# Optimization experiments

Measured on AMD Instinct MI355X. Metric: run time of the kernel, lower is better.

Reference implementation:

```python
import jax, jax.numpy as jnp
import numpy as np

NUM_EXPERTS = 64
TOP_K = 8
N_TOKENS = 131072  # batch*seq


def setup_inputs() -> dict:
    key = jax.random.key(0)
    k1, k2 = jax.random.split(key)
    top_scores = jax.random.uniform(k1, (N_TOKENS, TOP_K), dtype=jnp.float32)
    selected_experts_indices = jax.random.randint(
        k2, (N_TOKENS, TOP_K), 0, NUM_EXPERTS, dtype=jnp.int64
    )
    return {"top_scores": top_scores,
            "selected_experts_indices": selected_experts_indices}


def reference(top_scores, selected_experts_indices):
    flat_experts = selected_experts_indices.reshape(-1)          # (N*K,)
    # histogram of expert assignments (torch.histc with integer bins)
    num_tokens_per_expert = jnp.bincount(flat_experts, length=NUM_EXPERTS)
    # stable counting-sort permutation by expert id
    token_indices_experts_sorted = jnp.argsort(flat_experts, stable=True)
    top_scores_experts_sorted = top_scores.reshape(-1)[token_indices_experts_sorted]
    token_indices_experts_sorted = token_indices_experts_sorted // TOP_K
    return (top_scores_experts_sorted,
            token_indices_experts_sorted,
            num_tokens_per_expert)
```

## Files before the change

kernel.cpp:

```cpp
#include <hip/hip_runtime.h>

typedef unsigned int u32;
typedef unsigned long long u64;

#define NEXP    64
#define NB      256
#define EPB     4096
#define TPB     1024
#define WAVES   16
#define ROUNDS  4
#define LROWS   (NB / WAVES)
#define FLAG    0xC0000000u

__device__ __forceinline__ u64 matchmask(int val, int target) {
    u64 m = ~0ull;
#pragma unroll
    for (int b = 0; b < 6; ++b) {
        const u64 bl = __ballot((val >> b) & 1);
        m &= ((target >> b) & 1) ? bl : ~bl;
    }
    return m;
}

__device__ __forceinline__ u32 ld_agent(const u32* p) {
    return __hip_atomic_load(p, __ATOMIC_RELAXED, __HIP_MEMORY_SCOPE_AGENT);
}

__global__ __launch_bounds__(TPB) void k_fused(
        const float* __restrict__ scores,
        const int*   __restrict__ experts,
        u32*         __restrict__ sshist,
        float* __restrict__ out_scores,
        float* __restrict__ out_idx,
        float* __restrict__ out_counts) {
    __shared__ u32 h[WAVES][NEXP];
    __shared__ u32 cnt[WAVES][NEXP];
    __shared__ u32 Pp[WAVES][NEXP], Tp[WAVES][NEXP];
    __shared__ u32 gadj[NEXP];
    __shared__ u64 pair[EPB];

    const int t = threadIdx.x, lane = t & 63, s = t >> 6, b = blockIdx.x;
    const int wbase = b * EPB + s * (ROUNDS * 64);

    int e[ROUNDS];
#pragma unroll
    for (int r = 0; r < ROUNDS; ++r) e[r] = experts[wbase + r * 64 + lane];
    float sc[ROUNDS];
#pragma unroll
    for (int r = 0; r < ROUNDS; ++r) sc[r] = scores[wbase + r * 64 + lane];

    u32 hc = 0;
#pragma unroll
    for (int r = 0; r < ROUNDS; ++r) hc += (u32)__popcll(matchmask(e[r], lane));
    h[s][lane] = hc;
    __syncthreads();

    if (t < NEXP) {
        u32 H = 0;
#pragma unroll
        for (int w = 0; w < WAVES; ++w) H += h[w][t];
        __hip_atomic_store(&sshist[b * NEXP + t], H | FLAG,
                           __ATOMIC_RELAXED, __HIP_MEMORY_SCOPE_AGENT);
    }

    u32 pv[LROWS];
#pragma unroll
    for (int k = 0; k < LROWS; ++k)
        pv[k] = ld_agent(&sshist[(s * LROWS + k) * NEXP + lane]);

    for (;;) {
        bool done = true;
#pragma unroll
        for (int k = 0; k < LROWS; ++k) {
            if ((pv[k] & FLAG) != FLAG) {
                pv[k] = ld_agent(&sshist[(s * LROWS + k) * NEXP + lane]);
                if ((pv[k] & FLAG) != FLAG) done = false;
            }
        }
        if (done) break;
    }

    u32 pall = 0, plt = 0;
#pragma unroll
    for (int k = 0; k < LROWS; ++k) {
        const int row = s * LROWS + k;
        const u32 x = pv[k] & 0xFFFFu;
        pall += x;
        if (row < b) plt += x;
    }
    Pp[s][lane] = plt;
    Tp[s][lane] = pall;
    __syncthreads();

    if (t < NEXP) {
        u32 P = 0, T = 0;
#pragma unroll
        for (int w = 0; w < WAVES; ++w) { P += Pp[w][t]; T += Tp[w][t]; }
        u32 x = T;
#pragma unroll
        for (int d = 1; d < 64; d <<= 1) {
            const u32 y = __shfl_up(x, d);
            if (lane >= d) x += y;
        }
        const u32 base = x - T;

        u32 hw[WAVES];
#pragma unroll
        for (int w = 0; w < WAVES; ++w) hw[w] = h[w][t];
        u32 H = 0;
#pragma unroll
        for (int w = 0; w < WAVES; ++w) H += hw[w];
        u32 z = H;
#pragma unroll
        for (int d = 1; d < 64; d <<= 1) {
            const u32 y = __shfl_up(z, d);
            if (lane >= d) z += y;
        }
        const u32 lex = z - H;
        u32 run = lex;
#pragma unroll
        for (int w = 0; w < WAVES; ++w) { cnt[w][t] = run; run += hw[w]; }
        gadj[t] = base + P - lex;
        if (b == 0) out_counts[t] = (float)T;
    }
    __syncthreads();

#pragma unroll
    for (int r = 0; r < ROUNDS; ++r) {
        const int i = wbase + r * 64 + lane;
        const int ee = e[r];
        const u64 m = matchmask(ee, ee);
        const u32 lower = (u32)__popcll(m & ((1ull << lane) - 1ull));
        const u32 slot = cnt[s][ee] + lower;
        pair[slot] = ((u64)__float_as_uint(sc[r]) << 32)
                   | ((u32)(i >> 3) << 6) | (u32)ee;
        if (lower == 0) cnt[s][ee] += (u32)__popcll(m);
    }
    __syncthreads();

#pragma unroll
    for (int r = 0; r < ROUNDS; ++r) {
        const int j = r * TPB + t;
        const u64 v = pair[j];
        const u32 lo = (u32)v;
        const u32 dst = gadj[lo & 63u] + (u32)j;
        out_scores[dst] = __uint_as_float((u32)(v >> 32));
        out_idx[dst]    = (float)(lo >> 6);
    }
}

extern "C" void kernel_launch(void* const* d_in, const int* in_sizes, int n_in,
                              void* d_out, int out_size, void* d_ws, size_t ws_size,
                              hipStream_t stream) {
    const float* top_scores = (const float*)d_in[0];
    const int*   experts    = (const int*)d_in[1];

    const int M = in_sizes[0];

    u32* sshist = (u32*)d_ws;

    float* out = (float*)d_out;

    k_fused<<<NB, TPB, 0, stream>>>(top_scores, experts, sshist,
                                    out, out + M, out + 2 * (size_t)M);
}
```

Measured before the change: 14.55 us.

## Vectorize loads, reuse ballots, compute prefix per-wave to drop shared tables and barriers

```diff
diff --git a/kernel.cpp b/kernel.cpp
--- a/kernel.cpp
+++ b/kernel.cpp
@@ -8,22 +8,21 @@
 #define EPB     4096
 #define TPB     1024
 #define WAVES   16
-#define ROUNDS  4
 #define LROWS   (NB / WAVES)
 #define FLAG    0xC0000000u
 
-__device__ __forceinline__ u64 matchmask(int val, int target) {
-    u64 m = ~0ull;
-#pragma unroll
-    for (int b = 0; b < 6; ++b) {
-        const u64 bl = __ballot((val >> b) & 1);
-        m &= ((target >> b) & 1) ? bl : ~bl;
-    }
-    return m;
+__device__ __forceinline__ u32 ld_agent(const u32* p) {
+    return __hip_atomic_load(p, __ATOMIC_RELAXED, __HIP_MEMORY_SCOPE_AGENT);
 }
 
-__device__ __forceinline__ u32 ld_agent(const u32* p) {
-    return __hip_atomic_load(p, __ATOMIC_RELAXED, __HIP_MEMORY_SCOPE_AGENT);
+__device__ __forceinline__ u64 msk(const u64* bl, int target) {
+    u64 m = (target & 1)  ? bl[0] : ~bl[0];
+    m &=    (target & 2)  ? bl[1] : ~bl[1];
+    m &=    (target & 4)  ? bl[2] : ~bl[2];
+    m &=    (target & 8)  ? bl[3] : ~bl[3];
+    m &=    (target & 16) ? bl[4] : ~bl[4];
+    m &=    (target & 32) ? bl[5] : ~bl[5];
+    return m;
 }
 
 __global__ __launch_bounds__(TPB) void k_fused(
@@ -34,24 +33,32 @@
         float* __restrict__ out_idx,
         float* __restrict__ out_counts) {
     __shared__ u32 h[WAVES][NEXP];
-    __shared__ u32 cnt[WAVES][NEXP];
     __shared__ u32 Pp[WAVES][NEXP], Tp[WAVES][NEXP];
-    __shared__ u32 gadj[NEXP];
     __shared__ u64 pair[EPB];
 
     const int t = threadIdx.x, lane = t & 63, s = t >> 6, b = blockIdx.x;
-    const int wbase = b * EPB + s * (ROUNDS * 64);
+    const int mybase = b * EPB + s * 256 + lane * 4;
 
-    int e[ROUNDS];
+    const int4   ev = ((const int4*)experts)[mybase >> 2];
+    u32 pv[LROWS];
 #pragma unroll
-    for (int r = 0; r < ROUNDS; ++r) e[r] = experts[wbase + r * 64 + lane];
-    float sc[ROUNDS];
+    for (int k = 0; k < LROWS; ++k)
+        pv[k] = ld_agent(&sshist[(s * LROWS + k) * NEXP + lane]);
+    const float4 fv = ((const float4*)scores)[mybase >> 2];
+
+    const int   e4[4] = {ev.x, ev.y, ev.z, ev.w};
+    const float f4[4] = {fv.x, fv.y, fv.z, fv.w};
+
+    u64 bl[4][6];
 #pragma unroll
-    for (int r = 0; r < ROUNDS; ++r) sc[r] = scores[wbase + r * 64 + lane];
+    for (int j = 0; j < 4; ++j)
+#pragma unroll
+        for (int bb = 0; bb < 6; ++bb)
+            bl[j][bb] = __ballot((e4[j] >> bb) & 1);
 
     u32 hc = 0;
 #pragma unroll
-    for (int r = 0; r < ROUNDS; ++r) hc += (u32)__popcll(matchmask(e[r], lane));
+    for (int j = 0; j < 4; ++j) hc += (u32)__popcll(msk(bl[j], lane));
     h[s][lane] = hc;
     __syncthreads();
 
@@ -62,11 +69,6 @@
         __hip_atomic_store(&sshist[b * NEXP + t], H | FLAG,
                            __ATOMIC_RELAXED, __HIP_MEMORY_SCOPE_AGENT);
     }
-
-    u32 pv[LROWS];
-#pragma unroll
-    for (int k = 0; k < LROWS; ++k)
-        pv[k] = ld_agent(&sshist[(s * LROWS + k) * NEXP + lane]);
 
     for (;;) {
         bool done = true;
@@ -92,58 +94,56 @@
     Tp[s][lane] = pall;
     __syncthreads();
 
-    if (t < NEXP) {
-        u32 P = 0, T = 0;
+    u32 P = 0, T = 0, H = 0, hw_pre = 0;
 #pragma unroll
-        for (int w = 0; w < WAVES; ++w) { P += Pp[w][t]; T += Tp[w][t]; }
-        u32 x = T;
+    for (int w = 0; w < WAVES; ++w) {
+        const u32 hv = h[w][lane];
+        P += Pp[w][lane];
+        T += Tp[w][lane];
+        H += hv;
+        if (w < s) hw_pre += hv;
+    }
+    u32 x = T;
 #pragma unroll
-        for (int d = 1; d < 64; d <<= 1) {
-            const u32 y = __shfl_up(x, d);
-            if (lane >= d) x += y;
+    for (int d = 1; d < 64; d <<= 1) {
+        const u32 y = __shfl_up(x, d);
+        if (lane >= d) x += y;
+    }
+    const u32 base = x - T;
+    u32 z = H;
+#pragma unroll
+    for (int d = 1; d < 64; d <<= 1) {
+        const u32 y = __shfl_up(z, d);
+        if (lane >= d) z += y;
+    }
+    const u32 lex   = z - H;
+    const u32 cseed = lex + hw_pre;
+    const u32 gadj  = base + P - lex;
+    if (b == 0 && t < NEXP) out_counts[t] = (float)T;
+
+    const u64 lt = (1ull << lane) - 1ull;
+    const u64 le = lt | (1ull << lane);
+#pragma unroll
+    for (int j = 0; j < 4; ++j) {
+        u32 r = 0;
+#pragma unroll
+        for (int jp = 0; jp < 4; ++jp) {
+            const u64 m = msk(bl[jp], e4[j]);
+            r += (u32)__popcll(m & (jp < j ? le : lt));
         }
-        const u32 base = x - T;
-
-        u32 hw[WAVES];
-#pragma unroll
-        for (int w = 0; w < WAVES; ++w) hw[w] = h[w][t];
-        u32 H = 0;
-#pragma unroll
-        for (int w = 0; w < WAVES; ++w) H += hw[w];
-        u32 z = H;
-#pragma unroll
-        for (int d = 1; d < 64; d <<= 1) {
-            const u32 y = __shfl_up(z, d);
-            if (lane >= d) z += y;
-        }
-        const u32 lex = z - H;
-        u32 run = lex;
-#pragma unroll
-        for (int w = 0; w < WAVES; ++w) { cnt[w][t] = run; run += hw[w]; }
-        gadj[t] = base + P - lex;
-        if (b == 0) out_counts[t] = (float)T;
+        const u32 slot = (u32)__shfl((int)cseed, e4[j]) + r;
+        const u32 gi = (u32)(mybase + j);
+        pair[slot] = ((u64)__float_as_uint(f4[j]) << 32)
+                   | ((gi >> 3) << 6) | (u32)e4[j];
     }
     __syncthreads();
 
 #pragma unroll
-    for (int r = 0; r < ROUNDS; ++r) {
-        const int i = wbase + r * 64 + lane;
-        const int ee = e[r];
-        const u64 m = matchmask(ee, ee);
-        const u32 lower = (u32)__popcll(m & ((1ull << lane) - 1ull));
-        const u32 slot = cnt[s][ee] + lower;
-        pair[slot] = ((u64)__float_as_uint(sc[r]) << 32)
-                   | ((u32)(i >> 3) << 6) | (u32)ee;
-        if (lower == 0) cnt[s][ee] += (u32)__popcll(m);
-    }
-    __syncthreads();
-
-#pragma unroll
-    for (int r = 0; r < ROUNDS; ++r) {
+    for (int r = 0; r < 4; ++r) {
         const int j = r * TPB + t;
         const u64 v = pair[j];
         const u32 lo = (u32)v;
-        const u32 dst = gadj[lo & 63u] + (u32)j;
+        const u32 dst = (u32)__shfl((int)gadj, (int)(lo & 63u)) + (u32)j;
         out_scores[dst] = __uint_as_float((u32)(v >> 32));
         out_idx[dst]    = (float)(lo >> 6);
     }
```

Result: slower. 15.91 us (+9.3%).
